# Kernel tuning notes

Hardware: AMD Instinct MI355X
Metric: run time of the kernel (lower is better)

Reference implementation:

```python
import jax, jax.numpy as jnp
import numpy as np

N_TOKENS = 100000
CUT = [0, 20000, 50000, 100000]  # cutoff_ends
D = 1024


def setup_inputs() -> dict:
    key = jax.random.key(0)
    ks = jax.random.split(key, 12)
    B, S = 2, 1024
    hidden = jax.random.normal(ks[0], (B, S, D), dtype=jnp.float32)
    target = jax.random.randint(ks[1], (B, S), 0, N_TOKENS, dtype=jnp.int64)
    s = 0.02
    # cluster 0 (shortlist) + cluster projection head
    w0 = jax.random.normal(ks[2], (20000, 1024), dtype=jnp.float32) * s
    b0 = jnp.zeros((20000,), jnp.float32)
    cluster_w = jax.random.normal(ks[3], (2, 1024), dtype=jnp.float32) * s  # n_clusters=2
    cluster_b = jnp.zeros((2,), jnp.float32)
    proj0 = jax.random.normal(ks[4], (1024, 1024), dtype=jnp.float32) * s  # d_proj x d_emb_0
    # tail cluster 1: d_emb_1 = 1024 // 4 = 256, vocab slice 20000..50000
    w1 = jax.random.normal(ks[5], (30000, 256), dtype=jnp.float32) * s
    b1 = jnp.zeros((30000,), jnp.float32)
    proj1 = jax.random.normal(ks[6], (1024, 256), dtype=jnp.float32) * s
    # tail cluster 2: d_emb_2 = 1024 // 16 = 64, vocab slice 50000..100000
    w2 = jax.random.normal(ks[7], (50000, 64), dtype=jnp.float32) * s
    b2 = jnp.zeros((50000,), jnp.float32)
    proj2 = jax.random.normal(ks[8], (1024, 64), dtype=jnp.float32) * s
    return {"hidden": hidden, "target": target,
            "w0": w0, "b0": b0, "cluster_w": cluster_w, "cluster_b": cluster_b, "proj0": proj0,
            "w1": w1, "b1": b1, "proj1": proj1,
            "w2": w2, "b2": b2, "proj2": proj2}


def reference(hidden, target, w0, b0, cluster_w, cluster_b, proj0,
              w1, b1, proj1, w2, b2, proj2):
    tgt_shape = target.shape
    h = hidden.reshape(-1, D)            # [N, d_proj]
    t = target.reshape(-1)               # [N]

    # head: shortlist logits + cluster logits, via low-rank projection
    head_w = jnp.concatenate([w0, cluster_w], axis=0)   # [20002, 1024]
    head_b = jnp.concatenate([b0, cluster_b], axis=0)
    head_logit = (h @ proj0) @ head_w.T + head_b        # [N, 20002]
    head_lp = jax.nn.log_softmax(head_logit, axis=1)

    nll = jnp.zeros(t.shape, h.dtype)

    # cluster 0 (shortlist): logprob is head_lp at the target id
    m0 = t < CUT[1]
    idx0 = jnp.clip(t, 0, CUT[1] - 1)
    lp0 = jnp.take_along_axis(head_lp, idx0[:, None], axis=1)[:, 0]
    nll = jnp.where(m0, -lp0, nll)

    # tail clusters. NOTE: faithful to original quirk head_logprob[:, -i]
    tails = [(CUT[1], CUT[2], w1, b1, proj1), (CUT[2], CUT[3], w2, b2, proj2)]
    for i, (left, right, w, b, p) in enumerate(tails, start=1):
        m = (t >= left) & (t < right)
        tail_logit = (h @ p) @ w.T + b                  # [N, right-left]
        tail_lp = jax.nn.log_softmax(tail_logit, axis=1)
        ti = jnp.clip(t - left, 0, right - left - 1)
        lp = head_lp[:, -i] + jnp.take_along_axis(tail_lp, ti[:, None], axis=1)[:, 0]
        nll = jnp.where(m, -lp, nll)

    return nll.reshape(tgt_shape)
```

## Files before the change

### kernel.cpp

```cpp
#include <hip/hip_runtime.h>
#include <cstdint>
#include <cstddef>

#define DEV static __device__ __forceinline__

typedef __attribute__((ext_vector_type(8))) short bf16x8_t;
typedef __attribute__((ext_vector_type(4))) float f32x4_t;

DEV unsigned short f2bf(float f) {
  union { float f; unsigned u; } v; v.f = f;
  unsigned r = v.u + 0x7fffu + ((v.u >> 16) & 1u);
  return (unsigned short)(r >> 16);
}

DEV void gl_lds16(const void* g, void* l) {
  __builtin_amdgcn_global_load_lds(
      (const __attribute__((address_space(1))) void*)g,
      (__attribute__((address_space(3))) void*)l,
      16, 0, 0);
}

__global__ __launch_bounds__(256)
void prep_k(const int* __restrict__ target,
            int* __restrict__ idx1, int* __restrict__ pos1,
            int* __restrict__ idx2, int* __restrict__ pos2,
            int* __restrict__ cnts,
            const float* __restrict__ p0, const float* __restrict__ p1,
            const float* __restrict__ p2, unsigned short* __restrict__ pAll,
            const float* __restrict__ s0, unsigned short* __restrict__ d0, int n0,
            const float* __restrict__ s1, unsigned short* __restrict__ d1, int n1,
            const float* __restrict__ s2, unsigned short* __restrict__ d2, int n2,
            const float* __restrict__ s3, unsigned short* __restrict__ d3, int n3,
            const float* __restrict__ s4, unsigned short* __restrict__ d4, int n4) {
  const int bid = blockIdx.x;
  const int tid = threadIdx.x;
  if (bid == 0) {
    __shared__ int c1, c2;
    if (tid == 0) { c1 = 0; c2 = 0; }
    __syncthreads();
    for (int i = tid; i < 2048; i += 256) {
      int t = target[i];
      if (t >= 20000 && t < 50000) {
        int p = atomicAdd(&c1, 1); idx1[p] = i; pos1[i] = p;
      } else if (t >= 50000) {
        int p = atomicAdd(&c2, 1); idx2[p] = i; pos2[i] = p;
      }
    }
    __syncthreads();
    if (tid == 0) { cnts[0] = c1; cnts[1] = c2; }
    return;
  }
  if (bid <= 1344) {
    __shared__ float tile[32][33];
    int b = bid - 1;
    const float* src; unsigned short* dst; int C, bx, by;
    if (b < 1024)      { src = p0; dst = pAll;               C = 1024; bx = b % 32; by = b / 32; }
    else if (b < 1280) { int q = b - 1024; src = p1; dst = pAll + 1024 * 1024; C = 256; bx = q % 8; by = q / 8; }
    else               { int q = b - 1280; src = p2; dst = pAll + 1280 * 1024; C = 64;  bx = q % 2; by = q / 2; }
    const int R = 1024;
    int tx = tid & 31, ty = tid >> 5;
    int c0 = bx * 32, r0 = by * 32;
    for (int yy = ty; yy < 32; yy += 8)
      tile[yy][tx] = src[(size_t)(r0 + yy) * C + (c0 + tx)];
    __syncthreads();
    for (int yy = ty; yy < 32; yy += 8)
      dst[(size_t)(c0 + yy) * R + (r0 + tx)] = f2bf(tile[tx][yy]);
    return;
  }
  int j = (bid - 1345) * 256 + tid;
  const float* s; unsigned short* d;
  if (j < n0) { s = s0; d = d0; }
  else { j -= n0;
    if (j < n1) { s = s1; d = d1; }
    else { j -= n1;
      if (j < n2) { s = s2; d = d2; }
      else { j -= n2;
        if (j < n3) { s = s3; d = d3; }
        else { j -= n3; if (j >= n4) return; s = s4; d = d4; }
      }
    }
  }
  float4 f = ((const float4*)s)[j];
  ushort4 o;
  o.x = f2bf(f.x); o.y = f2bf(f.y); o.z = f2bf(f.z); o.w = f2bf(f.w);
  ((ushort4*)d)[j] = o;
}

__global__ __launch_bounds__(256)
void proj_gemm_k(const unsigned short* __restrict__ A,
                 const unsigned short* __restrict__ W,
                 unsigned short* __restrict__ Cout) {
  __shared__ __align__(16) unsigned short As[128 * 32];
  __shared__ __align__(16) unsigned short Bs[128 * 32];
  const int K = 1024, V = 1344;
  const int tm = blockIdx.x, tn = blockIdx.y;
  const int m0 = tm * 128, n0 = tn * 128;
  const int tid = threadIdx.x, wid = tid >> 6, lane = tid & 63;
  const int quad = lane >> 4, l16 = lane & 15;
  const int wr = wid >> 1, wc = wid & 1;

  f32x4_t acc[4][4];
  const f32x4_t zero4 = {0.f, 0.f, 0.f, 0.f};
#pragma unroll
  for (int i = 0; i < 4; ++i)
#pragma unroll
    for (int j = 0; j < 4; ++j) acc[i][j] = zero4;

  const int srow = wid * 32 + (lane >> 2);
  const int skk  = (lane & 3) * 8;
  const unsigned short* Ap0 = A + (size_t)(m0 + srow) * K + skk;
  const unsigned short* Ap1 = A + (size_t)(m0 + srow + 16) * K + skk;
  int wrow0 = n0 + srow;      if (wrow0 > V - 1) wrow0 = V - 1;
  int wrow1 = n0 + srow + 16; if (wrow1 > V - 1) wrow1 = V - 1;
  const unsigned short* Wp0 = W + (size_t)wrow0 * K + skk;
  const unsigned short* Wp1 = W + (size_t)wrow1 * K + skk;
  unsigned short* Asw = As + wid * 1024;
  unsigned short* Bsw = Bs + wid * 1024;

  for (int k0 = 0; k0 < K; k0 += 32) {
    gl_lds16(Ap0, Asw);
    gl_lds16(Ap1, Asw + 512);
    gl_lds16(Wp0, Bsw);
    gl_lds16(Wp1, Bsw + 512);
    Ap0 += 32; Ap1 += 32; Wp0 += 32; Wp1 += 32;
    __syncthreads();
    bf16x8_t af[4], bfr[4];
#pragma unroll
    for (int i = 0; i < 4; ++i)
      af[i] = *(const bf16x8_t*)(As + (size_t)(wr * 64 + i * 16 + l16) * 32 + quad * 8);
#pragma unroll
    for (int j = 0; j < 4; ++j)
      bfr[j] = *(const bf16x8_t*)(Bs + (size_t)(wc * 64 + j * 16 + l16) * 32 + quad * 8);
#pragma unroll
    for (int i = 0; i < 4; ++i)
#pragma unroll
      for (int j = 0; j < 4; ++j)
        acc[i][j] = __builtin_amdgcn_mfma_f32_16x16x32_bf16(af[i], bfr[j], acc[i][j], 0, 0, 0);
    __syncthreads();
  }
#pragma unroll
  for (int i = 0; i < 4; ++i)
#pragma unroll
    for (int j = 0; j < 4; ++j) {
      const int n = n0 + wc * 64 + j * 16 + l16;
      if (n < V) {
#pragma unroll
        for (int r = 0; r < 4; ++r) {
          const int m = m0 + wr * 64 + i * 16 + quad * 4 + r;
          Cout[(size_t)m * V + n] = f2bf(acc[i][j][r]);
        }
      }
    }
}


#define SBAR() __builtin_amdgcn_s_barrier()

#define STA(BUF, HALF, KT)                                                    \
  {                                                                           \
    const unsigned short* g_ = aB0 + (size_t)(HALF) * (128 * 1344) + (KT) * 64; \
    char* d_ = (char*)SA[BUF][HALF] + ldsw;                                   \
    gl_lds16(g_, d_);                                                         \
    gl_lds16(g_ + 64 * 1344, d_ + 8192);                                      \
  }

#define STB(BUF, HALF, KT)                                                    \
  {                                                                           \
    char* d_ = (char*)SB[BUF][HALF] + ldsw;                                   \
    gl_lds16(bP##HALF##0 + (KT) * 64, d_);                                    \
    gl_lds16(bP##HALF##1 + (KT) * 64, d_ + 8192);                             \
  }

#define MMQ(mb, nb, BB)                                                       \
  {                                                                           \
    _Pragma("unroll") for (int mi = 0; mi < 4; ++mi) {                        \
      _Pragma("unroll") for (int nj = 0; nj < 2; ++nj) {                      \
        acc[(mb) + mi][(nb) + nj] = __builtin_amdgcn_mfma_f32_16x16x32_bf16(  \
            Af[0][mi], BB[0][nj], acc[(mb) + mi][(nb) + nj], 0, 0, 0);        \
        acc[(mb) + mi][(nb) + nj] = __builtin_amdgcn_mfma_f32_16x16x32_bf16(  \
            Af[1][mi], BB[1][nj], acc[(mb) + mi][(nb) + nj], 0, 0, 0);        \
      }                                                                       \
    }                                                                         \
  }

#define PH(D_, E_, KTV)                                                       \
  {                                                                           \
    const int kt_ = (KTV);                                                    \
    const int t1_ = (kt_ + 1 > 15) ? 15 : (kt_ + 1);                          \
    const int t2_ = (kt_ + 2 > 15) ? 15 : (kt_ + 2);                          \
              \
    _Pragma("unroll") for (int mi = 0; mi < 4; ++mi) {                        \
      Af[0][mi] = *(const bf16x8_t*)(pa##D_##a + mi * 2048);                  \
      Af[1][mi] = *(const bf16x8_t*)(pa##D_##b + mi * 2048);                  \
    }                                                                         \
    _Pragma("unroll") for (int nj = 0; nj < 2; ++nj) {                        \
      Bh[0][nj] = *(const bf16x8_t*)(pb##D_##a + (2 + nj) * 2048);            \
      Bh[1][nj] = *(const bf16x8_t*)(pb##D_##b + (2 + nj) * 2048);            \
    }                                                                         \
    STB(E_, 1, t1_);                                                          \
    __builtin_amdgcn_s_setprio(1); MMQ(0, 0, Bl); __builtin_amdgcn_s_setprio(0); \
    SBAR();                                                                   \
              \
    __builtin_amdgcn_s_setprio(1); MMQ(0, 2, Bh); __builtin_amdgcn_s_setprio(0); \
    _Pragma("unroll") for (int mi = 0; mi < 4; ++mi) {                        \
      Af[0][mi] = *(const bf16x8_t*)(pa##D_##a + (4 + mi) * 2048);            \
      Af[1][mi] = *(const bf16x8_t*)(pa##D_##b + (4 + mi) * 2048);            \
    }                                                                         \
    STA(E_, 1, t1_);                                                          \
    SBAR();                                                                   \
               \
    STB(D_, 0, t2_);                                                          \
    __builtin_amdgcn_s_setprio(1); MMQ(4, 0, Bl); __builtin_amdgcn_s_setprio(0); \
    asm volatile("s_waitcnt vmcnt(2)" ::: "memory");                          \
    SBAR();                                                                   \
           \
    STA(D_, 0, t2_);                                                          \
    _Pragma("unroll") for (int nj = 0; nj < 2; ++nj) {                        \
      Bl[0][nj] = *(const bf16x8_t*)(pb##E_##a + nj * 2048);                  \
      Bl[1][nj] = *(const bf16x8_t*)(pb##E_##b + nj * 2048);                  \
    }                                                                         \
    __builtin_amdgcn_s_setprio(1); MMQ(4, 2, Bh); __builtin_amdgcn_s_setprio(0); \
    SBAR();                                                                   \
  }

#define PROLOGUE6()                                                           \
  { STB(0, 0, 0); STA(0, 0, 0); STB(0, 1, 0); STA(0, 1, 0);                   \
    STB(1, 0, 1); STA(1, 0, 1); }

__global__ __launch_bounds__(512, 2)
void head256_k(const unsigned short* __restrict__ Pall,
               const unsigned short* __restrict__ w0b,
               const float* __restrict__ b0, const float* __restrict__ cb,
               float* __restrict__ part0, float* __restrict__ g0,
               float* __restrict__ cg, const int* __restrict__ target) {
  __shared__ __align__(16) unsigned short SA[2][2][8192];
  __shared__ __align__(16) unsigned short SB[2][2][8192];

  const int V = 20002;
  const int bid = blockIdx.x;
  const int orig = (bid & 7) * 79 + (bid >> 3);
  const int mt = orig & 7, stripe = orig >> 3;
  const int m0 = mt * 256, n0 = stripe * 256;

  const int tid = threadIdx.x;
  const int wid = tid >> 6, lane = tid & 63;
  const int quad = lane >> 4, l16 = lane & 15;
  const int wr = wid >> 2, wc = wid & 3;

  const int r0  = tid >> 3;
  const int ibh = ((tid & 7) ^ (r0 & 7)) << 3;

  const unsigned short* aB0 = Pall + (size_t)(m0 + r0) * 1344 + ibh;
  int br00 = n0 + r0;            if (br00 > V - 1) br00 = V - 1;
  int br01 = n0 + r0 + 64;       if (br01 > V - 1) br01 = V - 1;
  int br10 = n0 + 128 + r0;      if (br10 > V - 1) br10 = V - 1;
  int br11 = n0 + 128 + r0 + 64; if (br11 > V - 1) br11 = V - 1;
  const unsigned short* bP00 = w0b + (size_t)br00 * 1024 + ibh;
  const unsigned short* bP01 = w0b + (size_t)br01 * 1024 + ibh;
  const unsigned short* bP10 = w0b + (size_t)br10 * 1024 + ibh;
  const unsigned short* bP11 = w0b + (size_t)br11 * 1024 + ibh;

  const int ldsw = wid * 1024;

  const int aoff0 = l16 * 128 + ((quad ^ (l16 & 3)) << 4) + (((l16 >> 2) & 1) << 6);
  const int aoff1 = aoff0 ^ 64;
  const char* pa0a = (const char*)SA[0][wr] + aoff0;
  const char* pa0b = (const char*)SA[0][wr] + aoff1;
  const char* pa1a = (const char*)SA[1][wr] + aoff0;
  const char* pa1b = (const char*)SA[1][wr] + aoff1;
  const char* pb0a = (const char*)SB[0][wc >> 1] + (wc & 1) * 8192 + aoff0;
  const char* pb0b = (const char*)SB[0][wc >> 1] + (wc & 1) * 8192 + aoff1;
  const char* pb1a = (const char*)SB[1][wc >> 1] + (wc & 1) * 8192 + aoff0;
  const char* pb1b = (const char*)SB[1][wc >> 1] + (wc & 1) * 8192 + aoff1;

  f32x4_t acc[8][4];
  const f32x4_t zero4 = {0.f, 0.f, 0.f, 0.f};
#pragma unroll
  for (int i = 0; i < 8; ++i)
#pragma unroll
    for (int j = 0; j < 4; ++j) acc[i][j] = zero4;

  bf16x8_t Af[2][4];
  bf16x8_t Bl[2][2];
  bf16x8_t Bh[2][2];

  PROLOGUE6();
  asm volatile("s_waitcnt vmcnt(4)" ::: "memory");
  SBAR();
#pragma unroll
  for (int nj = 0; nj < 2; ++nj) {
    Bl[0][nj] = *(const bf16x8_t*)(pb0a + nj * 2048);
    Bl[1][nj] = *(const bf16x8_t*)(pb0b + nj * 2048);
  }

#pragma unroll 1
  for (int ktp = 0; ktp < 8; ++ktp) {
    const int kt0 = 2 * ktp;
    PH(0, 1, kt0);
    PH(1, 0, kt0 + 1);
  }

  asm volatile("s_waitcnt vmcnt(0) lgkmcnt(0)" ::: "memory");
  SBAR();

  int nj[4]; float bj[4];
#pragma unroll
  for (int j = 0; j < 4; ++j) {
    nj[j] = n0 + wc * 64 + j * 16 + l16;
    bj[j] = (nj[j] < 20000) ? b0[nj[j]] : ((nj[j] < V) ? cb[nj[j] - 20000] : 0.f);
  }
  float* redf = (float*)&SA[0][0][0];
#pragma unroll
  for (int i = 0; i < 8; ++i) {
#pragma unroll
    for (int r = 0; r < 4; ++r) {
      const int rloc = i * 16 + quad * 4 + r;
      const int token = m0 + wr * 128 + rloc;
      float v[4], sum = 0.f;
#pragma unroll
      for (int j = 0; j < 4; ++j) {
        v[j] = acc[i][j][r] + bj[j];
        if (nj[j] < V) sum += __expf(v[j]);
      }
#pragma unroll
      for (int off = 1; off < 16; off <<= 1)
        sum += __shfl_xor(sum, off, 64);
      if (l16 == 0) redf[(wr * 4 + wc) * 128 + rloc] = sum;
      const int t = target[token];
      const int gi = (t < 19999) ? t : 19999;
#pragma unroll
      for (int j = 0; j < 4; ++j) {
        if (nj[j] == gi) g0[token] = v[j];
        if (nj[j] == 20000) cg[2 * token]     = v[j];
        if (nj[j] == 20001) cg[2 * token + 1] = v[j];
      }
    }
  }
  __syncthreads();
  if (tid < 256) {
    const int wrr = tid >> 7, rr = tid & 127;
    const float s = redf[(wrr * 4 + 0) * 128 + rr] + redf[(wrr * 4 + 1) * 128 + rr]
                  + redf[(wrr * 4 + 2) * 128 + rr] + redf[(wrr * 4 + 3) * 128 + rr];
    part0[(size_t)(m0 + tid) * 79 + stripe] = s;
  }
}

#undef PH
#undef MMQ
#undef STA
#undef STB
#undef PROLOGUE6
#undef SBAR

template <int KT>
__global__ __launch_bounds__(256, 1)
void tail_stripe_k(const unsigned short* __restrict__ A, int ldA,
                   const unsigned short* __restrict__ W,
                   const float* __restrict__ bias, int V, int ntiles,
                   const int* __restrict__ rowidx,
                   const int* __restrict__ cnt_ptr,
                   float* __restrict__ partials,
                   float* __restrict__ gathered,
                   const int* __restrict__ target, int glo) {
  constexpr int NC = KT / 32;
  __shared__ __align__(16) unsigned short Ws[NC][128 * 32];
  __shared__ __align__(16) unsigned short As[NC][128 * 32];
  __shared__ float red[2][128];

  const int tn = blockIdx.x, n0 = tn * 128;
  const int Meff = *cnt_ptr;
  const int tid = threadIdx.x, wid = tid >> 6, lane = tid & 63;
  const int quad = lane >> 4, l16 = lane & 15;
  const int wr = wid >> 1, wc = wid & 1;
  const int srow = wid * 32 + (lane >> 2);
  const int skk  = (lane & 3) * 8;

  int wrow0 = n0 + srow;      if (wrow0 > V - 1) wrow0 = V - 1;
  int wrow1 = n0 + srow + 16; if (wrow1 > V - 1) wrow1 = V - 1;
#pragma unroll
  for (int c = 0; c < NC; ++c) {
    gl_lds16(W + (size_t)wrow0 * KT + c * 32 + skk, Ws[c] + wid * 1024);
    gl_lds16(W + (size_t)wrow1 * KT + c * 32 + skk, Ws[c] + wid * 1024 + 512);
  }

  int nj[4]; float bj[4];
#pragma unroll
  for (int j = 0; j < 4; ++j) {
    nj[j] = n0 + wc * 64 + j * 16 + l16;
    bj[j] = (nj[j] < V) ? bias[nj[j]] : 0.f;
  }

  const int nm = (Meff + 127) >> 7;
  for (int m = 0; m < nm; ++m) {
    const int m0 = m * 128;
    int ar0 = m0 + srow;      if (ar0 > Meff - 1) ar0 = Meff - 1;
    int ar1 = m0 + srow + 16; if (ar1 > Meff - 1) ar1 = Meff - 1;
    ar0 = rowidx[ar0]; ar1 = rowidx[ar1];
#pragma unroll
    for (int c = 0; c < NC; ++c) {
      gl_lds16(A + (size_t)ar0 * ldA + c * 32 + skk, As[c] + wid * 1024);
      gl_lds16(A + (size_t)ar1 * ldA + c * 32 + skk, As[c] + wid * 1024 + 512);
    }
    __syncthreads();

    f32x4_t acc[4][4];
    const f32x4_t zero4 = {0.f, 0.f, 0.f, 0.f};
#pragma unroll
    for (int i = 0; i < 4; ++i)
#pragma unroll
      for (int j = 0; j < 4; ++j) acc[i][j] = zero4;
#pragma unroll
    for (int c = 0; c < NC; ++c) {
      bf16x8_t af[4], bfr[4];
#pragma unroll
      for (int i = 0; i < 4; ++i)
        af[i] = *(const bf16x8_t*)(As[c] + (size_t)(wr * 64 + i * 16 + l16) * 32 + quad * 8);
#pragma unroll
      for (int j = 0; j < 4; ++j)
        bfr[j] = *(const bf16x8_t*)(Ws[c] + (size_t)(wc * 64 + j * 16 + l16) * 32 + quad * 8);
#pragma unroll
      for (int i = 0; i < 4; ++i)
#pragma unroll
        for (int j = 0; j < 4; ++j)
          acc[i][j] = __builtin_amdgcn_mfma_f32_16x16x32_bf16(af[i], bfr[j], acc[i][j], 0, 0, 0);
    }

#pragma unroll
    for (int i = 0; i < 4; ++i) {
#pragma unroll
      for (int r = 0; r < 4; ++r) {
        const int row = wr * 64 + i * 16 + quad * 4 + r;
        const int gr = m0 + row;
        const int grc = (gr < Meff) ? gr : (Meff - 1);
        const int token = rowidx[grc];
        float v[4], sum = 0.f;
#pragma unroll
        for (int j = 0; j < 4; ++j) {
          v[j] = acc[i][j][r] + bj[j];
          if (nj[j] < V) sum += __expf(v[j]);
        }
#pragma unroll
        for (int off = 1; off < 16; off <<= 1)
          sum += __shfl_xor(sum, off, 64);
        if (l16 == 0) red[wc][row] = sum;
        const int gi = target[token] - glo;
#pragma unroll
        for (int j = 0; j < 4; ++j)
          if (nj[j] == gi) gathered[token] = v[j];
      }
    }
    __syncthreads();
    if (tid < 128 && (m0 + tid) < Meff)
      partials[(size_t)(m0 + tid) * ntiles + tn] = red[0][tid] + red[1][tid];
  }
}

__global__ __launch_bounds__(256)
void combine_k(const float* __restrict__ part0,
               const float* __restrict__ part1, int nt1,
               const float* __restrict__ part2, int nt2,
               const float* __restrict__ g0, const float* __restrict__ g1,
               const float* __restrict__ g2, const float* __restrict__ cg,
               const int* __restrict__ pos1, const int* __restrict__ pos2,
               const int* __restrict__ target, float* __restrict__ out) {
  const int w = threadIdx.x >> 6, lane = threadIdx.x & 63;
  const int token = blockIdx.x * 4 + w;
  const int t = target[token];

  float S = 0.f;
  for (int i = lane; i < 79; i += 64)
    S += part0[(size_t)token * 79 + i];
#pragma unroll
  for (int off = 1; off < 64; off <<= 1)
    S += __shfl_xor(S, off, 64);
  const float lse_head = __logf(S);

  float res;
  if (t < 20000) {
    res = lse_head - g0[token];
  } else {
    const float* pt; int nt; float gv, ch; int row;
    if (t < 50000) { pt = part1; nt = nt1; gv = g1[token]; ch = cg[2 * token + 1]; row = pos1[token]; }
    else           { pt = part2; nt = nt2; gv = g2[token]; ch = cg[2 * token];     row = pos2[token]; }
    float S2 = 0.f;
    for (int i = lane; i < nt; i += 64)
      S2 += pt[(size_t)row * nt + i];
#pragma unroll
    for (int off = 1; off < 64; off <<= 1)
      S2 += __shfl_xor(S2, off, 64);
    float lse_t = __logf(S2);
    res = -((ch - lse_head) + (gv - lse_t));
  }
  if (lane == 0) out[token] = res;
}

extern "C" void kernel_launch(void* const* d_in, const int* in_sizes, int n_in,
                              void* d_out, int out_size, void* d_ws, size_t ws_size,
                              hipStream_t stream) {
  (void)in_sizes; (void)n_in; (void)out_size; (void)ws_size;
  const float* hidden = (const float*)d_in[0];
  const int*   target = (const int*)d_in[1];
  const float* w0     = (const float*)d_in[2];
  const float* b0     = (const float*)d_in[3];
  const float* cw     = (const float*)d_in[4];
  const float* cb     = (const float*)d_in[5];
  const float* proj0  = (const float*)d_in[6];
  const float* w1     = (const float*)d_in[7];
  const float* b1     = (const float*)d_in[8];
  const float* proj1  = (const float*)d_in[9];
  const float* w2     = (const float*)d_in[10];
  const float* b2     = (const float*)d_in[11];
  const float* proj2  = (const float*)d_in[12];
  float* out = (float*)d_out;

  const int NT1 = 235, NT2 = 391;

  char* p = (char*)d_ws;
  auto alloc = [&](size_t bytes) {
    char* r = p; p += (bytes + 255) & ~(size_t)255; return r;
  };
  unsigned short* Hb   = (unsigned short*)alloc(2048ull * 1024 * 2);
  unsigned short* pAll = (unsigned short*)alloc(1344ull * 1024 * 2);
  unsigned short* w0b  = (unsigned short*)alloc(20002ull * 1024 * 2);
  unsigned short* w1b  = (unsigned short*)alloc(30000ull * 256 * 2);
  unsigned short* w2b  = (unsigned short*)alloc(50000ull * 64 * 2);
  unsigned short* Pall = (unsigned short*)alloc(2048ull * 1344 * 2);
  float* part0 = (float*)alloc(2048ull * 79 * 4);
  float* part1 = (float*)alloc(2048ull * NT1 * 4);
  float* part2 = (float*)alloc(2048ull * NT2 * 4);
  float* g0 = (float*)alloc(2048 * 4);
  float* g1 = (float*)alloc(2048 * 4);
  float* g2 = (float*)alloc(2048 * 4);
  float* cg = (float*)alloc(2048 * 2 * 4);
  int* idx1 = (int*)alloc(2048 * 4);
  int* pos1 = (int*)alloc(2048 * 4);
  int* idx2 = (int*)alloc(2048 * 4);
  int* pos2 = (int*)alloc(2048 * 4);
  int* cnts = (int*)alloc(2 * 4);

  const int c_h = 2048 * 1024 / 4, c_w0 = 20000 * 1024 / 4, c_cw = 2048 / 4,
            c_w1 = 30000 * 256 / 4, c_w2 = 50000 * 64 / 4;
  const int ctot = c_h + c_w0 + c_cw + c_w1 + c_w2;
  const int nb_cast = (ctot + 255) / 256;
  prep_k<<<1 + 1344 + nb_cast, 256, 0, stream>>>(
      target, idx1, pos1, idx2, pos2, cnts,
      proj0, proj1, proj2, pAll,
      hidden, Hb, c_h,
      w0, w0b, c_w0,
      cw, w0b + 20000ull * 1024, c_cw,
      w1, w1b, c_w1,
      w2, w2b, c_w2);

  proj_gemm_k<<<dim3(16, 11), 256, 0, stream>>>(Hb, pAll, Pall);

  head256_k<<<632, 512, 0, stream>>>(Pall, w0b, b0, cb, part0, g0, cg, target);

  tail_stripe_k<256><<<NT1, 256, 0, stream>>>(
      Pall + 1024, 1344, w1b, b1, 30000, NT1, idx1, cnts + 0,
      part1, g1, target, 20000);
  tail_stripe_k<64><<<NT2, 256, 0, stream>>>(
      Pall + 1280, 1344, w2b, b2, 50000, NT2, idx2, cnts + 1,
      part2, g2, target, 50000);

  combine_k<<<512, 256, 0, stream>>>(part0, part1, NT1, part2, NT2,
      g0, g1, g2, cg, pos1, pos2, target, out);
}
```

Before: 425.4 us.

## Fuse head and both tail logit kernels into one launch with shared LDS union

Merges the head kernel and the two tail-cluster kernels into a single launch that dispatches on block index, with all three bodies sharing one raw LDS buffer. The aim is to remove two kernel boundaries and let tail blocks fill the head GEMM's partial last wave. In exchange, tail blocks now run with 512 threads (half idle) and reserve the full 132 KB of LDS, so fewer tail blocks can be resident per CU. The block-index offset into the second tail region is hardcoded to match NT1.

```diff
diff --git a/kernel.cpp b/kernel.cpp
--- a/kernel.cpp
+++ b/kernel.cpp
@@ -227,17 +227,18 @@
   { STB(0, 0, 0); STA(0, 0, 0); STB(0, 1, 0); STA(0, 1, 0);                   \
     STB(1, 0, 1); STA(1, 0, 1); }
 
-__global__ __launch_bounds__(512, 2)
-void head256_k(const unsigned short* __restrict__ Pall,
-               const unsigned short* __restrict__ w0b,
-               const float* __restrict__ b0, const float* __restrict__ cb,
-               float* __restrict__ part0, float* __restrict__ g0,
-               float* __restrict__ cg, const int* __restrict__ target) {
-  __shared__ __align__(16) unsigned short SA[2][2][8192];
-  __shared__ __align__(16) unsigned short SB[2][2][8192];
+typedef unsigned short lds_half_t[2][8192];
+
+DEV void head_body(char* UB, int bid,
+                   const unsigned short* __restrict__ Pall,
+                   const unsigned short* __restrict__ w0b,
+                   const float* __restrict__ b0, const float* __restrict__ cb,
+                   float* __restrict__ part0, float* __restrict__ g0,
+                   float* __restrict__ cg, const int* __restrict__ target) {
+  lds_half_t* SA = (lds_half_t*)UB;
+  lds_half_t* SB = (lds_half_t*)(UB + 65536);
 
   const int V = 20002;
-  const int bid = blockIdx.x;
   const int orig = (bid & 7) * 79 + (bid >> 3);
   const int mt = orig & 7, stripe = orig >> 3;
   const int m0 = mt * 256, n0 = stripe * 256;
@@ -309,7 +310,7 @@
     nj[j] = n0 + wc * 64 + j * 16 + l16;
     bj[j] = (nj[j] < 20000) ? b0[nj[j]] : ((nj[j] < V) ? cb[nj[j] - 20000] : 0.f);
   }
-  float* redf = (float*)&SA[0][0][0];
+  float* redf = (float*)UB;
 #pragma unroll
   for (int i = 0; i < 8; ++i) {
 #pragma unroll
@@ -353,8 +354,8 @@
 #undef SBAR
 
 template <int KT>
-__global__ __launch_bounds__(256, 1)
-void tail_stripe_k(const unsigned short* __restrict__ A, int ldA,
+DEV void tail_body(char* UB, int tn,
+                   const unsigned short* __restrict__ A, int ldA,
                    const unsigned short* __restrict__ W,
                    const float* __restrict__ bias, int V, int ntiles,
                    const int* __restrict__ rowidx,
@@ -363,13 +364,15 @@
                    float* __restrict__ gathered,
                    const int* __restrict__ target, int glo) {
   constexpr int NC = KT / 32;
-  __shared__ __align__(16) unsigned short Ws[NC][128 * 32];
-  __shared__ __align__(16) unsigned short As[NC][128 * 32];
-  __shared__ float red[2][128];
-
-  const int tn = blockIdx.x, n0 = tn * 128;
+  unsigned short (*Ws)[128 * 32] = (unsigned short (*)[128 * 32])UB;
+  unsigned short (*As)[128 * 32] = (unsigned short (*)[128 * 32])(UB + NC * 8192);
+  float (*red)[128] = (float (*)[128])(UB + 2 * NC * 8192);
+
+  const int n0 = tn * 128;
   const int Meff = *cnt_ptr;
-  const int tid = threadIdx.x, wid = tid >> 6, lane = tid & 63;
+  const int tid = threadIdx.x;
+  const bool act = tid < 256;
+  const int wid = tid >> 6, lane = tid & 63;
   const int quad = lane >> 4, l16 = lane & 15;
   const int wr = wid >> 1, wc = wid & 1;
   const int srow = wid * 32 + (lane >> 2);
@@ -377,81 +380,113 @@
 
   int wrow0 = n0 + srow;      if (wrow0 > V - 1) wrow0 = V - 1;
   int wrow1 = n0 + srow + 16; if (wrow1 > V - 1) wrow1 = V - 1;
-#pragma unroll
-  for (int c = 0; c < NC; ++c) {
-    gl_lds16(W + (size_t)wrow0 * KT + c * 32 + skk, Ws[c] + wid * 1024);
-    gl_lds16(W + (size_t)wrow1 * KT + c * 32 + skk, Ws[c] + wid * 1024 + 512);
+  if (act) {
+#pragma unroll
+    for (int c = 0; c < NC; ++c) {
+      gl_lds16(W + (size_t)wrow0 * KT + c * 32 + skk, Ws[c] + wid * 1024);
+      gl_lds16(W + (size_t)wrow1 * KT + c * 32 + skk, Ws[c] + wid * 1024 + 512);
+    }
   }
 
   int nj[4]; float bj[4];
 #pragma unroll
   for (int j = 0; j < 4; ++j) {
     nj[j] = n0 + wc * 64 + j * 16 + l16;
-    bj[j] = (nj[j] < V) ? bias[nj[j]] : 0.f;
+    bj[j] = (act && nj[j] < V) ? bias[nj[j]] : 0.f;
   }
 
   const int nm = (Meff + 127) >> 7;
   for (int m = 0; m < nm; ++m) {
     const int m0 = m * 128;
-    int ar0 = m0 + srow;      if (ar0 > Meff - 1) ar0 = Meff - 1;
-    int ar1 = m0 + srow + 16; if (ar1 > Meff - 1) ar1 = Meff - 1;
-    ar0 = rowidx[ar0]; ar1 = rowidx[ar1];
-#pragma unroll
-    for (int c = 0; c < NC; ++c) {
-      gl_lds16(A + (size_t)ar0 * ldA + c * 32 + skk, As[c] + wid * 1024);
-      gl_lds16(A + (size_t)ar1 * ldA + c * 32 + skk, As[c] + wid * 1024 + 512);
-    }
-    __syncthreads();
-
-    f32x4_t acc[4][4];
-    const f32x4_t zero4 = {0.f, 0.f, 0.f, 0.f};
-#pragma unroll
-    for (int i = 0; i < 4; ++i)
-#pragma unroll
-      for (int j = 0; j < 4; ++j) acc[i][j] = zero4;
-#pragma unroll
-    for (int c = 0; c < NC; ++c) {
-      bf16x8_t af[4], bfr[4];
+    if (act) {
+      int ar0 = m0 + srow;      if (ar0 > Meff - 1) ar0 = Meff - 1;
+      int ar1 = m0 + srow + 16; if (ar1 > Meff - 1) ar1 = Meff - 1;
+      ar0 = rowidx[ar0]; ar1 = rowidx[ar1];
+#pragma unroll
+      for (int c = 0; c < NC; ++c) {
+        gl_lds16(A + (size_t)ar0 * ldA + c * 32 + skk, As[c] + wid * 1024);
+        gl_lds16(A + (size_t)ar1 * ldA + c * 32 + skk, As[c] + wid * 1024 + 512);
+      }
+    }
+    __syncthreads();
+
+    if (act) {
+      f32x4_t acc[4][4];
+      const f32x4_t zero4 = {0.f, 0.f, 0.f, 0.f};
 #pragma unroll
       for (int i = 0; i < 4; ++i)
-        af[i] = *(const bf16x8_t*)(As[c] + (size_t)(wr * 64 + i * 16 + l16) * 32 + quad * 8);
-#pragma unroll
-      for (int j = 0; j < 4; ++j)
-        bfr[j] = *(const bf16x8_t*)(Ws[c] + (size_t)(wc * 64 + j * 16 + l16) * 32 + quad * 8);
-#pragma unroll
-      for (int i = 0; i < 4; ++i)
+#pragma unroll
+        for (int j = 0; j < 4; ++j) acc[i][j] = zero4;
+#pragma unroll
+      for (int c = 0; c < NC; ++c) {
+        bf16x8_t af[4], bfr[4];
+#pragma unroll
+        for (int i = 0; i < 4; ++i)
+          af[i] = *(const bf16x8_t*)(As[c] + (size_t)(wr * 64 + i * 16 + l16) * 32 + quad * 8);
 #pragma unroll
         for (int j = 0; j < 4; ++j)
-          acc[i][j] = __builtin_amdgcn_mfma_f32_16x16x32_bf16(af[i], bfr[j], acc[i][j], 0, 0, 0);
-    }
-
-#pragma unroll
-    for (int i = 0; i < 4; ++i) {
-#pragma unroll
-      for (int r = 0; r < 4; ++r) {
-        const int row = wr * 64 + i * 16 + quad * 4 + r;
-        const int gr = m0 + row;
-        const int grc = (gr < Meff) ? gr : (Meff - 1);
-        const int token = rowidx[grc];
-        float v[4], sum = 0.f;
-#pragma unroll
-        for (int j = 0; j < 4; ++j) {
-          v[j] = acc[i][j][r] + bj[j];
-          if (nj[j] < V) sum += __expf(v[j]);
+          bfr[j] = *(const bf16x8_t*)(Ws[c] + (size_t)(wc * 64 + j * 16 + l16) * 32 + quad * 8);
+#pragma unroll
+        for (int i = 0; i < 4; ++i)
+#pragma unroll
+          for (int j = 0; j < 4; ++j)
+            acc[i][j] = __builtin_amdgcn_mfma_f32_16x16x32_bf16(af[i], bfr[j], acc[i][j], 0, 0, 0);
+      }
+
+#pragma unroll
+      for (int i = 0; i < 4; ++i) {
+#pragma unroll
+        for (int r = 0; r < 4; ++r) {
+          const int row = wr * 64 + i * 16 + quad * 4 + r;
+          const int gr = m0 + row;
+          const int grc = (gr < Meff) ? gr : (Meff - 1);
+          const int token = rowidx[grc];
+          float v[4], sum = 0.f;
+#pragma unroll
+          for (int j = 0; j < 4; ++j) {
+            v[j] = acc[i][j][r] + bj[j];
+            if (nj[j] < V) sum += __expf(v[j]);
+          }
+#pragma unroll
+          for (int off = 1; off < 16; off <<= 1)
+            sum += __shfl_xor(sum, off, 64);
+          if (l16 == 0) red[wc][row] = sum;
+          const int gi = target[token] - glo;
+#pragma unroll
+          for (int j = 0; j < 4; ++j)
+            if (nj[j] == gi) gathered[token] = v[j];
         }
-#pragma unroll
-        for (int off = 1; off < 16; off <<= 1)
-          sum += __shfl_xor(sum, off, 64);
-        if (l16 == 0) red[wc][row] = sum;
-        const int gi = target[token] - glo;
-#pragma unroll
-        for (int j = 0; j < 4; ++j)
-          if (nj[j] == gi) gathered[token] = v[j];
       }
     }
     __syncthreads();
     if (tid < 128 && (m0 + tid) < Meff)
       partials[(size_t)(m0 + tid) * ntiles + tn] = red[0][tid] + red[1][tid];
+  }
+}
+
+__global__ __launch_bounds__(512, 2)
+void fused_k(const unsigned short* __restrict__ Pall,
+             const unsigned short* __restrict__ w0b,
+             const float* __restrict__ b0, const float* __restrict__ cb,
+             float* __restrict__ part0, float* __restrict__ g0,
+             float* __restrict__ cg, const int* __restrict__ target,
+             const unsigned short* __restrict__ w1b, const float* __restrict__ b1,
+             const int* __restrict__ idx1, const int* __restrict__ cnt1,
+             float* __restrict__ part1, float* __restrict__ g1,
+             const unsigned short* __restrict__ w2b, const float* __restrict__ b2,
+             const int* __restrict__ idx2, const int* __restrict__ cnt2,
+             float* __restrict__ part2, float* __restrict__ g2,
+             int nt1, int nt2) {
+  __shared__ __align__(16) char UB[132096];
+  const int bid = blockIdx.x;
+  if (bid < 632) {
+    head_body(UB, bid, Pall, w0b, b0, cb, part0, g0, cg, target);
+  } else if (bid < 632 + 235) {
+    tail_body<256>(UB, bid - 632, Pall + 1024, 1344, w1b, b1, 30000, nt1,
+                   idx1, cnt1, part1, g1, target, 20000);
+  } else {
+    tail_body<64>(UB, bid - 867, Pall + 1280, 1344, w2b, b2, 50000, nt2,
+                  idx2, cnt2, part2, g2, target, 50000);
   }
 }
 
@@ -553,14 +588,11 @@
 
   proj_gemm_k<<<dim3(16, 11), 256, 0, stream>>>(Hb, pAll, Pall);
 
-  head256_k<<<632, 512, 0, stream>>>(Pall, w0b, b0, cb, part0, g0, cg, target);
-
-  tail_stripe_k<256><<<NT1, 256, 0, stream>>>(
-      Pall + 1024, 1344, w1b, b1, 30000, NT1, idx1, cnts + 0,
-      part1, g1, target, 20000);
-  tail_stripe_k<64><<<NT2, 256, 0, stream>>>(
-      Pall + 1280, 1344, w2b, b2, 50000, NT2, idx2, cnts + 1,
-      part2, g2, target, 50000);
+  fused_k<<<632 + NT1 + NT2, 512, 0, stream>>>(
+      Pall, w0b, b0, cb, part0, g0, cg, target,
+      w1b, b1, idx1, cnts + 0, part1, g1,
+      w2b, b2, idx2, cnts + 1, part2, g2,
+      NT1, NT2);
 
   combine_k<<<512, 256, 0, stream>>>(part0, part1, NT1, part2, NT2,
       g0, g1, g2, cg, pos1, pos2, target, out);
```

New measurement: 418.3 us. About the same (-1.6%).
